# Performance work log

Measured on AMD Instinct MI355X. Metric: run time of the kernel, lower is better.

Reference implementation:

```python
import jax, jax.numpy as jnp
import numpy as np

NUM_HEADS = 16
D_MODEL = 1024
HEAD_DIM = D_MODEL // NUM_HEADS
SCALE = float(np.sqrt(HEAD_DIM))  # NOTE: original multiplies q by sqrt(head_dim)
EPS = 1e-5


def layernorm(x, g, b):
    # LayerNorm over last dim (head_dim), learnable affine
    mu = jnp.mean(x, axis=-1, keepdims=True)
    var = jnp.mean(jnp.square(x - mu), axis=-1, keepdims=True)
    return (x - mu) * jax.lax.rsqrt(var + EPS) * g + b


def setup_inputs() -> dict:
    key = jax.random.key(0)
    ks = jax.random.split(key, 8)
    B, Nq, Nc = 2, 2048, 2048
    s = 0.02
    return {
        "x_query": jax.random.normal(ks[0], (B, Nq, D_MODEL), jnp.float32),
        "x_context": jax.random.normal(ks[1], (B, Nc, D_MODEL), jnp.float32),
        "Wq": jax.random.normal(ks[2], (D_MODEL, D_MODEL), jnp.float32) * s,
        "Wkv": jax.random.normal(ks[3], (D_MODEL, 2 * D_MODEL), jnp.float32) * s,
        "Wp": jax.random.normal(ks[4], (D_MODEL, D_MODEL), jnp.float32) * s,
        "bp": jnp.zeros((D_MODEL,), jnp.float32),
        "ln_g": jnp.ones((HEAD_DIM,), jnp.float32),
        "ln_b": jnp.zeros((HEAD_DIM,), jnp.float32),
    }


def reference(x_query, x_context, Wq, Wkv, Wp, bp, ln_g, ln_b):
    B, Nq, _ = x_query.shape
    Nc = x_context.shape[1]
    H, D = NUM_HEADS, HEAD_DIM
    # projections
    q = (x_query @ Wq).reshape(B, Nq, H, D).transpose(0, 2, 1, 3)  # b h n d
    kv = (x_context @ Wkv).reshape(B, Nc, 2, H, D)
    k = kv[:, :, 0].transpose(0, 2, 1, 3)  # b h n d
    v = kv[:, :, 1].transpose(0, 2, 1, 3)
    # QK-LayerNorm (shared params)
    q = layernorm(q, ln_g, ln_b)
    k = layernorm(k, ln_g, ln_b)
    # NOTE: faithful to source — q is MULTIPLIED by sqrt(head_dim)
    q = q * SCALE
    attn = jnp.einsum("bhqd,bhkd->bhqk", q, k)
    attn = jax.nn.softmax(attn, axis=-1)
    out = jnp.einsum("bhqk,bhkd->bhqd", attn, v)
    out = out.transpose(0, 2, 1, 3).reshape(B, Nq, H * D)
    return out @ Wp + bp
```

## Files before the change

### kernel.cpp

```cpp
#include <hip/hip_runtime.h>
#include <stdint.h>

#define NUM_HEADS 16
#define HEAD_DIM 64
#define D_MODEL 1024
#define SEQ 2048
#define BATCH 2

typedef unsigned short u16;
typedef _Float16 f16x8 __attribute__((ext_vector_type(8)));
typedef float f32x4 __attribute__((ext_vector_type(4)));

__device__ __forceinline__ u16 f2h(float f) {
    _Float16 h = (_Float16)f;
    return __builtin_bit_cast(u16, h);
}
__device__ __forceinline__ float h2f(u16 h) {
    return (float)__builtin_bit_cast(_Float16, h);
}
__device__ __forceinline__ uint32_t pkrtz(float a, float b) {
    return __builtin_bit_cast(uint32_t, __builtin_amdgcn_cvt_pkrtz(a, b));
}

__device__ __forceinline__ f16x8 ld8h(const u16* p) {
    return *reinterpret_cast<const f16x8*>(p);
}

__device__ __forceinline__ void gl_lds16(const void* g, void* l) {
    __builtin_amdgcn_global_load_lds(
        (const __attribute__((address_space(1))) void*)g,
        (__attribute__((address_space(3))) void*)l,
        16, 0, 0);
}

template <int CTRL>
__device__ __forceinline__ float dpp_mov(float x) {
    return __builtin_bit_cast(float,
        __builtin_amdgcn_update_dpp(0, __builtin_bit_cast(int, x), CTRL, 0xf, 0xf, true));
}
__device__ __forceinline__ float rowsum16(float x) {
    x += dpp_mov<0x121>(x);
    x += dpp_mov<0x122>(x);
    x += dpp_mov<0x124>(x);
    x += dpp_mov<0x128>(x);
    return x;
}

__global__ __launch_bounds__(256) void k_prep(const float* __restrict__ xq,
                                              const float* __restrict__ xc,
                                              const float* __restrict__ Wq,
                                              const float* __restrict__ Wkv,
                                              const float* __restrict__ Wp,
                                              u16* __restrict__ xq16,
                                              u16* __restrict__ xc16,
                                              u16* __restrict__ WqT16,
                                              u16* __restrict__ WkvT16,
                                              u16* __restrict__ WpT16) {
    __shared__ float tile[32][33];
    const int t = blockIdx.x;
    if (t < 8192) {
        int i = t * 256 + threadIdx.x;
        const float* src; u16* dst; int j;
        if (i < 1048576) { src = xq; dst = xq16; j = i; }
        else             { src = xc; dst = xc16; j = i - 1048576; }
        float4 v = reinterpret_cast<const float4*>(src)[j];
        ushort4 o;
        o.x = f2h(v.x); o.y = f2h(v.y); o.z = f2h(v.z); o.w = f2h(v.w);
        reinterpret_cast<ushort4*>(dst)[j] = o;
        return;
    }
    const float* W; u16* WT; int N, bi;
    if (t < 9216)       { W = Wq;  WT = WqT16;  N = 1024; bi = t - 8192; }
    else if (t < 11264) { W = Wkv; WT = WkvT16; N = 2048; bi = t - 9216; }
    else                { W = Wp;  WT = WpT16;  N = 1024; bi = t - 11264; }
    const int K = 1024;
    const int nb = N / 32;
    const int bn = (bi % nb) * 32, bk = (bi / nb) * 32;
    const int tx = threadIdx.x & 31;
    const int ty = threadIdx.x >> 5;
#pragma unroll
    for (int i = 0; i < 32; i += 8)
        tile[ty + i][tx] = W[(size_t)(bk + ty + i) * N + bn + tx];
    __syncthreads();
#pragma unroll
    for (int i = 0; i < 32; i += 8)
        WT[(size_t)(bn + ty + i) * K + bk + tx] = f2h(tile[tx][ty + i]);
}

__device__ __forceinline__ void gemm_mainloop_f16(const u16* __restrict__ A,
                                                  const u16* __restrict__ Bt,
                                                  u16* As, u16* Bs,
                                                  int tileM, int tileN, int K,
                                                  f32x4 acc[4][4]) {
    const int tid = threadIdx.x;
    const int lane = tid & 63;
    const int wv = tid >> 6;
    const int wm = wv >> 1, wn = wv & 1;
    const int quad = lane >> 4, l15 = lane & 15;

    const int c0 = tid, c1 = tid + 256;
    const u16* Ap0 = A + (size_t)(tileM + (c0 >> 2)) * K + (c0 & 3) * 8;
    const u16* Ap1 = A + (size_t)(tileM + (c1 >> 2)) * K + (c1 & 3) * 8;
    const u16* Bp0 = Bt + (size_t)(tileN + (c0 >> 2)) * K + (c0 & 3) * 8;
    const u16* Bp1 = Bt + (size_t)(tileN + (c1 >> 2)) * K + (c1 & 3) * 8;

    for (int k0 = 0; k0 < K; k0 += 32) {
        __syncthreads();
        gl_lds16(Ap0 + k0, &As[c0 * 8]);
        gl_lds16(Ap1 + k0, &As[c1 * 8]);
        gl_lds16(Bp0 + k0, &Bs[c0 * 8]);
        gl_lds16(Bp1 + k0, &Bs[c1 * 8]);
        __syncthreads();
        f16x8 af[4], bfr[4];
#pragma unroll
        for (int mi = 0; mi < 4; ++mi)
            af[mi] = ld8h(&As[(wm * 64 + mi * 16 + l15) * 32 + quad * 8]);
#pragma unroll
        for (int ni = 0; ni < 4; ++ni)
            bfr[ni] = ld8h(&Bs[(wn * 64 + ni * 16 + l15) * 32 + quad * 8]);
#pragma unroll
        for (int mi = 0; mi < 4; ++mi)
#pragma unroll
            for (int ni = 0; ni < 4; ++ni)
                acc[mi][ni] = __builtin_amdgcn_mfma_f32_16x16x32_f16(
                    af[mi], bfr[ni], acc[mi][ni], 0, 0, 0);
    }
}

#define ACC_INIT()                                                   \
    f32x4 acc[4][4];                                                 \
    _Pragma("unroll") for (int i = 0; i < 4; ++i)                    \
        _Pragma("unroll") for (int j = 0; j < 4; ++j)                \
            acc[i][j] = (f32x4){0.f, 0.f, 0.f, 0.f};

__global__ __launch_bounds__(256, 2) void k_proj_f16(const u16* __restrict__ xq16,
                                                     const u16* __restrict__ xc16,
                                                     const u16* __restrict__ WqT16,
                                                     const u16* __restrict__ WkvT16,
                                                     const float* __restrict__ lng,
                                                     const float* __restrict__ lnb,
                                                     u16* __restrict__ Qh_h,
                                                     u16* __restrict__ Qh_l,
                                                     u16* __restrict__ Kh,
                                                     u16* __restrict__ VT) {
    __shared__ __align__(16) u16 As[128 * 32];
    __shared__ __align__(16) u16 Bs[128 * 32];
    const int bx = blockIdx.x;
    const int tileM = blockIdx.y * 128;
    const int tid = threadIdx.x;
    const int lane = tid & 63;
    const int wv = tid >> 6;
    const int wm = wv >> 1, wn = wv & 1;
    const int quad = lane >> 4, l15 = lane & 15;
    ACC_INIT();

    if (bx < 16) {
        const bool isQ = bx < 8;
        const int tileN = (bx & 7) * 128;
        const u16* Axx = isQ ? xq16 : xc16;
        const u16* Bt  = isQ ? WqT16 : WkvT16;
        const float scl = isQ ? 8.0f : 1.0f;

        gemm_mainloop_f16(Axx, Bt, As, Bs, tileM, tileN, D_MODEL, acc);

        float gv[4], bv[4];
#pragma unroll
        for (int ni = 0; ni < 4; ++ni) { gv[ni] = lng[ni * 16 + l15]; bv[ni] = lnb[ni * 16 + l15]; }

#pragma unroll
        for (int mi = 0; mi < 4; ++mi) {
#pragma unroll
            for (int r = 0; r < 4; ++r) {
                float sum = 0.f, sq = 0.f;
#pragma unroll
                for (int ni = 0; ni < 4; ++ni) { float x = acc[mi][ni][r]; sum += x; sq += x * x; }
                sum = rowsum16(sum);
                sq  = rowsum16(sq);
                float mu = sum * (1.f / 64.f);
                float var = sq * (1.f / 64.f) - mu * mu;
                float rs = rsqrtf(var + 1e-5f);
                int m = tileM + wm * 64 + mi * 16 + quad * 4 + r;
                int bb = m >> 11, n = m & (SEQ - 1);
#pragma unroll
                for (int ni = 0; ni < 4; ++ni) {
                    int colg = tileN + wn * 64 + ni * 16 + l15;
                    int h = colg >> 6;
                    float y = ((acc[mi][ni][r] - mu) * rs * gv[ni] + bv[ni]) * scl;
                    size_t idx = (((size_t)bb * NUM_HEADS + h) * SEQ + n) * HEAD_DIM + (colg & 63);
                    u16 yh = f2h(y);
                    if (isQ) {
                        Qh_h[idx] = yh;
                        Qh_l[idx] = f2h(y - h2f(yh));
                    } else {
                        Kh[idx] = yh;
                    }
                }
            }
        }
    } else {
        const int tileN = D_MODEL + (bx - 16) * 128;
        gemm_mainloop_f16(xc16, WkvT16, As, Bs, tileM, tileN, D_MODEL, acc);
#pragma unroll
        for (int mi = 0; mi < 4; ++mi) {
            int m0 = tileM + wm * 64 + mi * 16 + quad * 4;
            int bb = m0 >> 11, n0 = m0 & (SEQ - 1);
#pragma unroll
            for (int ni = 0; ni < 4; ++ni) {
                int colg = tileN + wn * 64 + ni * 16 + l15 - D_MODEL;
                int h = colg >> 6, d = colg & 63;
                ushort4 o;
                o.x = f2h(acc[mi][ni][0]);
                o.y = f2h(acc[mi][ni][1]);
                o.z = f2h(acc[mi][ni][2]);
                o.w = f2h(acc[mi][ni][3]);
                *reinterpret_cast<ushort4*>(
                    &VT[(((size_t)bb * NUM_HEADS + h) * HEAD_DIM + d) * SEQ + n0]) = o;
            }
        }
    }
}

__global__ __launch_bounds__(256, 2) void k_gemm_out(const u16* __restrict__ A,
                                                     const u16* __restrict__ Bt,
                                                     const float* __restrict__ bp,
                                                     float* __restrict__ out) {
    __shared__ __align__(16) u16 As[128 * 32];
    __shared__ __align__(16) u16 Bs[128 * 32];
    const int tileM = blockIdx.y * 128, tileN = blockIdx.x * 128;
    const int tid = threadIdx.x;
    const int lane = tid & 63;
    const int wv = tid >> 6;
    const int wm = wv >> 1, wn = wv & 1;
    const int quad = lane >> 4, l15 = lane & 15;
    ACC_INIT();
    gemm_mainloop_f16(A, Bt, As, Bs, tileM, tileN, D_MODEL, acc);

    float bpv[4];
#pragma unroll
    for (int ni = 0; ni < 4; ++ni) bpv[ni] = bp[tileN + wn * 64 + ni * 16 + l15];
#pragma unroll
    for (int mi = 0; mi < 4; ++mi) {
#pragma unroll
        for (int r = 0; r < 4; ++r) {
            int m = tileM + wm * 64 + mi * 16 + quad * 4 + r;
#pragma unroll
            for (int ni = 0; ni < 4; ++ni) {
                int colg = tileN + wn * 64 + ni * 16 + l15;
                out[(size_t)m * D_MODEL + colg] = acc[mi][ni][r] + bpv[ni];
            }
        }
    }
}

__global__ __launch_bounds__(256) void k_attn(const u16* __restrict__ Qh_h,
                                              const u16* __restrict__ Qh_l,
                                              const u16* __restrict__ Kh,
                                              const u16* __restrict__ VT,
                                              u16* __restrict__ AO) {
    __shared__ __align__(16) u16 Ks[2 * 64 * 64];
    __shared__ __align__(16) u16 Vs[2 * 64 * 64];
    __shared__ __align__(16) u16 Ps[64 * 64];

    const int tid = threadIdx.x;
    const int lane = tid & 63;
    const int wv = tid >> 6;
    const int quad = lane >> 4, l15 = lane & 15;
    const int sw = l15 & 3;
    const int id = blockIdx.x;
    const int bh = (id & 7) | (((id >> 8) & 3) << 3);
    const int qt = (id >> 3) & 31;

    const size_t bh_off = (size_t)bh * SEQ * HEAD_DIM;
    const u16* Vbh = VT + (size_t)bh * HEAD_DIM * SEQ;

    f16x8 qfh[2], qfl[2];
#pragma unroll
    for (int kt = 0; kt < 2; ++kt) {
        size_t off = bh_off + (size_t)(qt * 64 + wv * 16 + l15) * HEAD_DIM + kt * 32 + quad * 8;
        qfh[kt] = ld8h(Qh_h + off);
        qfl[kt] = ld8h(Qh_l + off);
    }

    const int rr = lane >> 3;
    const int ss = lane & 7;
    const int cc = ss ^ rr;
    const int row0 = wv * 16 + rr;
    const u16* k0 = Kh + bh_off + (size_t)row0 * HEAD_DIM + cc * 8;
    const u16* v0 = Vbh + (size_t)row0 * SEQ + cc * 8;
    const int ldsW = (wv * 16) * 64;

    f32x4 acc_o[4];
    float m_i = -3.0e38f, l_i = 0.f;
#pragma unroll
    for (int ni = 0; ni < 4; ++ni) acc_o[ni] = (f32x4){0.f, 0.f, 0.f, 0.f};

    gl_lds16(k0,                &Ks[ldsW]);
    gl_lds16(k0 + 8 * HEAD_DIM, &Ks[ldsW + 8 * 64]);
    gl_lds16(v0,                &Vs[ldsW]);
    gl_lds16(v0 + 8 * SEQ,      &Vs[ldsW + 8 * 64]);

    const int psRow = (wv * 16 + l15) * 64;

    for (int j = 0; j < SEQ / 64; ++j) {
        __syncthreads();
        if (j + 1 < SEQ / 64) {
            const int nb = (j + 1) & 1;
            const size_t ko = (size_t)(j + 1) * 64 * HEAD_DIM;
            const int vo = (j + 1) * 64;
            gl_lds16(k0 + ko,                &Ks[nb * 4096 + ldsW]);
            gl_lds16(k0 + ko + 8 * HEAD_DIM, &Ks[nb * 4096 + ldsW + 8 * 64]);
            gl_lds16(v0 + vo,                &Vs[nb * 4096 + ldsW]);
            gl_lds16(v0 + vo + 8 * SEQ,      &Vs[nb * 4096 + ldsW + 8 * 64]);
        }
        const int bb = (j & 1) * 4096;

        f32x4 acc_s[4];
#pragma unroll
        for (int ni = 0; ni < 4; ++ni) acc_s[ni] = (f32x4){0.f, 0.f, 0.f, 0.f};
#pragma unroll
        for (int kt = 0; kt < 2; ++kt) {
            f16x8 kf[4];
#pragma unroll
            for (int ni = 0; ni < 4; ++ni) {
                int slot = (kt * 4 + quad) ^ (l15 & 7);
                kf[ni] = ld8h(&Ks[bb + (ni * 16 + l15) * 64 + slot * 8]);
            }
#pragma unroll
            for (int ni = 0; ni < 4; ++ni) {
                acc_s[ni] = __builtin_amdgcn_mfma_f32_16x16x32_f16(
                    kf[ni], qfh[kt], acc_s[ni], 0, 0, 0);
                acc_s[ni] = __builtin_amdgcn_mfma_f32_16x16x32_f16(
                    kf[ni], qfl[kt], acc_s[ni], 0, 0, 0);
            }
        }

        float mx = acc_s[0][0];
#pragma unroll
        for (int ni = 0; ni < 4; ++ni)
#pragma unroll
            for (int r = 0; r < 4; ++r) mx = fmaxf(mx, acc_s[ni][r]);
        mx = fmaxf(mx, __shfl_xor(mx, 16, 64));
        mx = fmaxf(mx, __shfl_xor(mx, 32, 64));
        float mnew = fmaxf(m_i, mx);
        float alpha = __expf(m_i - mnew);
        float sum = 0.f;
#pragma unroll
        for (int ni = 0; ni < 4; ++ni) {
            float p0 = __expf(acc_s[ni][0] - mnew);
            float p1 = __expf(acc_s[ni][1] - mnew);
            float p2 = __expf(acc_s[ni][2] - mnew);
            float p3 = __expf(acc_s[ni][3] - mnew);
            sum += (p0 + p1) + (p2 + p3);
            uint2 u;
            u.x = pkrtz(p0, p1);
            u.y = pkrtz(p2, p3);
            *reinterpret_cast<uint2*>(&Ps[psRow + ((ni ^ sw) * 16) + quad * 4]) = u;
        }
        sum += __shfl_xor(sum, 16, 64);
        sum += __shfl_xor(sum, 32, 64);
        m_i = mnew;
        l_i = l_i * alpha + sum;
#pragma unroll
        for (int ni = 0; ni < 4; ++ni) acc_o[ni] *= alpha;

#pragma unroll
        for (int kt = 0; kt < 2; ++kt) {
            int pchunk = (kt * 2 + (quad >> 1)) ^ sw;
            f16x8 pf = ld8h(&Ps[psRow + pchunk * 16 + (quad & 1) * 8]);
            f16x8 vf[4];
#pragma unroll
            for (int ni = 0; ni < 4; ++ni) {
                int slot = (kt * 4 + quad) ^ (l15 & 7);
                vf[ni] = ld8h(&Vs[bb + (ni * 16 + l15) * 64 + slot * 8]);
            }
#pragma unroll
            for (int ni = 0; ni < 4; ++ni)
                acc_o[ni] = __builtin_amdgcn_mfma_f32_16x16x32_f16(
                    vf[ni], pf, acc_o[ni], 0, 0, 0);
        }
    }

    const float inv = 1.0f / l_i;
#pragma unroll
    for (int ni = 0; ni < 4; ++ni) {
        uint2 u;
        u.x = pkrtz(acc_o[ni][0] * inv, acc_o[ni][1] * inv);
        u.y = pkrtz(acc_o[ni][2] * inv, acc_o[ni][3] * inv);
        *reinterpret_cast<uint2*>(&Ps[psRow + ((ni ^ sw) * 16) + quad * 4]) = u;
    }
    const int b = bh >> 4, h = bh & 15;
    const int qrow = qt * 64 + wv * 16 + l15;
    const int echunk = quad ^ sw;
    uint4 o0 = *reinterpret_cast<const uint4*>(&Ps[psRow + echunk * 16]);
    uint4 o1 = *reinterpret_cast<const uint4*>(&Ps[psRow + echunk * 16 + 8]);
    size_t outb = ((size_t)(b * SEQ + qrow)) * D_MODEL + h * 64 + quad * 16;
    *reinterpret_cast<uint4*>(&AO[outb])     = o0;
    *reinterpret_cast<uint4*>(&AO[outb + 8]) = o1;
}

extern "C" void kernel_launch(void* const* d_in, const int* in_sizes, int n_in,
                              void* d_out, int out_size, void* d_ws, size_t ws_size,
                              hipStream_t stream) {
    const float* xq  = (const float*)d_in[0];
    const float* xc  = (const float*)d_in[1];
    const float* Wq  = (const float*)d_in[2];
    const float* Wkv = (const float*)d_in[3];
    const float* Wp  = (const float*)d_in[4];
    const float* bp  = (const float*)d_in[5];
    const float* lng = (const float*)d_in[6];
    const float* lnb = (const float*)d_in[7];
    float* out = (float*)d_out;

    char* ws = (char*)d_ws;
    const size_t MB = 1 << 20;
    u16* xq16   = (u16*)(ws + 0 * MB);
    u16* xc16   = (u16*)(ws + 8 * MB);
    u16* WqT16  = (u16*)(ws + 16 * MB);
    u16* WkvT16 = (u16*)(ws + 18 * MB);
    u16* WpT16  = (u16*)(ws + 22 * MB);
    u16* Qh_h   = (u16*)(ws + 24 * MB);
    u16* Qh_l   = (u16*)(ws + 32 * MB);
    u16* Kh     = (u16*)(ws + 40 * MB);
    u16* VT     = (u16*)(ws + 48 * MB);
    u16* AO     = xq16;

    k_prep<<<12288, 256, 0, stream>>>(xq, xc, Wq, Wkv, Wp,
                                      xq16, xc16, WqT16, WkvT16, WpT16);
    k_proj_f16<<<dim3(24, 32), 256, 0, stream>>>(xq16, xc16, WqT16, WkvT16,
                                                 lng, lnb, Qh_h, Qh_l, Kh, VT);
    k_attn<<<1024, 256, 0, stream>>>(Qh_h, Qh_l, Kh, VT, AO);
    k_gemm_out<<<dim3(8, 32), 256, 0, stream>>>(AO, WpT16, bp, out);
}
```

Baseline: 258.0 us.

## Fold log2e into Q scale, use exp2, MFMA row sums, lazy rescale

Scales Q by sqrt(d)*log2(e) in the projection epilogue so the softmax can use raw exp2 instead of __expf. The row-sum of probabilities is now computed by an extra MFMA against a ones vector, replacing shuffle reductions. The output and running-sum rescale is skipped when no row maximum in the wave grew. The P-tile LDS write and read pattern gains an extra XOR swizzle to reduce bank conflicts. Together these aim to cut VALU and shuffle work in the attention inner loop, at the cost of an extra MFMA per k-step and a wave-wide branch.

Result: faster. 245.4 us (-4.9%).

```diff
diff --git a/kernel.cpp b/kernel.cpp
--- a/kernel.cpp
+++ b/kernel.cpp
@@ -20,6 +20,16 @@
 }
 __device__ __forceinline__ uint32_t pkrtz(float a, float b) {
     return __builtin_bit_cast(uint32_t, __builtin_amdgcn_cvt_pkrtz(a, b));
+}
+
+__device__ __forceinline__ float ex2(float x) {
+#if __has_builtin(__builtin_amdgcn_exp2f)
+    return __builtin_amdgcn_exp2f(x);
+#else
+    float r;
+    asm("v_exp_f32 %0, %1" : "=v"(r) : "v"(x));
+    return r;
+#endif
 }
 
 __device__ __forceinline__ f16x8 ld8h(const u16* p) {
@@ -159,7 +169,7 @@
         const int tileN = (bx & 7) * 128;
         const u16* Axx = isQ ? xq16 : xc16;
         const u16* Bt  = isQ ? WqT16 : WkvT16;
-        const float scl = isQ ? 8.0f : 1.0f;
+        const float scl = isQ ? 11.5415603294809528f : 1.0f;
 
         gemm_mainloop_f16(Axx, Bt, As, Bs, tileM, tileN, D_MODEL, acc);
 
@@ -266,6 +276,7 @@
     const int wv = tid >> 6;
     const int quad = lane >> 4, l15 = lane & 15;
     const int sw = l15 & 3;
+    const int w1 = (l15 >> 2) & 1;
     const int id = blockIdx.x;
     const int bh = (id & 7) | (((id >> 8) & 3) << 3);
     const int qt = (id >> 3) & 31;
@@ -280,6 +291,10 @@
         qfh[kt] = ld8h(Qh_h + off);
         qfl[kt] = ld8h(Qh_l + off);
     }
+
+    f16x8 ones;
+#pragma unroll
+    for (int i = 0; i < 8; ++i) ones[i] = (_Float16)1.0f;
 
     const int rr = lane >> 3;
     const int ss = lane & 7;
@@ -290,7 +305,8 @@
     const int ldsW = (wv * 16) * 64;
 
     f32x4 acc_o[4];
-    float m_i = -3.0e38f, l_i = 0.f;
+    f32x4 acc_l = (f32x4){0.f, 0.f, 0.f, 0.f};
+    float m_i = -3.0e38f;
 #pragma unroll
     for (int ni = 0; ni < 4; ++ni) acc_o[ni] = (f32x4){0.f, 0.f, 0.f, 0.f};
 
@@ -300,6 +316,7 @@
     gl_lds16(v0 + 8 * SEQ,      &Vs[ldsW + 8 * 64]);
 
     const int psRow = (wv * 16 + l15) * 64;
+    const int psW = psRow + (quad ^ (w1 << 1)) * 4;
 
     for (int j = 0; j < SEQ / 64; ++j) {
         __syncthreads();
@@ -334,39 +351,38 @@
             }
         }
 
-        float mx = acc_s[0][0];
+        float mn[4];
 #pragma unroll
         for (int ni = 0; ni < 4; ++ni)
-#pragma unroll
-            for (int r = 0; r < 4; ++r) mx = fmaxf(mx, acc_s[ni][r]);
+            mn[ni] = fmaxf(fmaxf(acc_s[ni][0], acc_s[ni][1]),
+                           fmaxf(acc_s[ni][2], acc_s[ni][3]));
+        float mx = fmaxf(fmaxf(mn[0], mn[1]), fmaxf(mn[2], mn[3]));
         mx = fmaxf(mx, __shfl_xor(mx, 16, 64));
         mx = fmaxf(mx, __shfl_xor(mx, 32, 64));
         float mnew = fmaxf(m_i, mx);
-        float alpha = __expf(m_i - mnew);
-        float sum = 0.f;
+        if (__any(mx > m_i)) {
+            float alpha = ex2(m_i - mnew);
+#pragma unroll
+            for (int ni = 0; ni < 4; ++ni) acc_o[ni] *= alpha;
+            acc_l[0] *= alpha;
+            m_i = mnew;
+        }
 #pragma unroll
         for (int ni = 0; ni < 4; ++ni) {
-            float p0 = __expf(acc_s[ni][0] - mnew);
-            float p1 = __expf(acc_s[ni][1] - mnew);
-            float p2 = __expf(acc_s[ni][2] - mnew);
-            float p3 = __expf(acc_s[ni][3] - mnew);
-            sum += (p0 + p1) + (p2 + p3);
+            float p0 = ex2(acc_s[ni][0] - mnew);
+            float p1 = ex2(acc_s[ni][1] - mnew);
+            float p2 = ex2(acc_s[ni][2] - mnew);
+            float p3 = ex2(acc_s[ni][3] - mnew);
             uint2 u;
             u.x = pkrtz(p0, p1);
             u.y = pkrtz(p2, p3);
-            *reinterpret_cast<uint2*>(&Ps[psRow + ((ni ^ sw) * 16) + quad * 4]) = u;
-        }
-        sum += __shfl_xor(sum, 16, 64);
-        sum += __shfl_xor(sum, 32, 64);
-        m_i = mnew;
-        l_i = l_i * alpha + sum;
-#pragma unroll
-        for (int ni = 0; ni < 4; ++ni) acc_o[ni] *= alpha;
+            *reinterpret_cast<uint2*>(&Ps[psW + ((ni ^ sw) * 16)]) = u;
+        }
 
 #pragma unroll
         for (int kt = 0; kt < 2; ++kt) {
             int pchunk = (kt * 2 + (quad >> 1)) ^ sw;
-            f16x8 pf = ld8h(&Ps[psRow + pchunk * 16 + (quad & 1) * 8]);
+            f16x8 pf = ld8h(&Ps[psRow + pchunk * 16 + (((quad & 1) ^ w1) * 8)]);
             f16x8 vf[4];
 #pragma unroll
             for (int ni = 0; ni < 4; ++ni) {
@@ -377,22 +393,24 @@
             for (int ni = 0; ni < 4; ++ni)
                 acc_o[ni] = __builtin_amdgcn_mfma_f32_16x16x32_f16(
                     vf[ni], pf, acc_o[ni], 0, 0, 0);
-        }
-    }
-
-    const float inv = 1.0f / l_i;
+            acc_l = __builtin_amdgcn_mfma_f32_16x16x32_f16(
+                ones, pf, acc_l, 0, 0, 0);
+        }
+    }
+
+    const float inv = 1.0f / acc_l[0];
 #pragma unroll
     for (int ni = 0; ni < 4; ++ni) {
         uint2 u;
         u.x = pkrtz(acc_o[ni][0] * inv, acc_o[ni][1] * inv);
         u.y = pkrtz(acc_o[ni][2] * inv, acc_o[ni][3] * inv);
-        *reinterpret_cast<uint2*>(&Ps[psRow + ((ni ^ sw) * 16) + quad * 4]) = u;
+        *reinterpret_cast<uint2*>(&Ps[psW + ((ni ^ sw) * 16)]) = u;
     }
     const int b = bh >> 4, h = bh & 15;
     const int qrow = qt * 64 + wv * 16 + l15;
     const int echunk = quad ^ sw;
-    uint4 o0 = *reinterpret_cast<const uint4*>(&Ps[psRow + echunk * 16]);
-    uint4 o1 = *reinterpret_cast<const uint4*>(&Ps[psRow + echunk * 16 + 8]);
+    uint4 o0 = *reinterpret_cast<const uint4*>(&Ps[psRow + echunk * 16 + w1 * 8]);
+    uint4 o1 = *reinterpret_cast<const uint4*>(&Ps[psRow + echunk * 16 + (1 - w1) * 8]);
     size_t outb = ((size_t)(b * SEQ + qrow)) * D_MODEL + h * 64 + quad * 16;
     *reinterpret_cast<uint4*>(&AO[outb])     = o0;
     *reinterpret_cast<uint4*>(&AO[outb + 8]) = o1;
```
